# Optimization experiments

Measured on AMD Instinct MI355X. Metric: run time of the kernel, lower is better.

Reference implementation:

```python
import jax, jax.numpy as jnp
import numpy as np

N_EMBD = 1024
N_HEAD = 16
HEAD_DIM = N_EMBD // N_HEAD


def setup_inputs() -> dict:
    key = jax.random.key(0)
    kx, kq, kk, kv, kp = jax.random.split(key, 5)
    B, S = 4, 2048
    x = jax.random.normal(kx, (B, S, N_EMBD), dtype=jnp.float32)
    # nn.Linear(n, n, bias=False): weight [out, in], y = x @ W.T
    s = 1.0 / np.sqrt(N_EMBD)
    Wq = jax.random.uniform(kq, (N_EMBD, N_EMBD), jnp.float32, -s, s)
    Wk = jax.random.uniform(kk, (N_EMBD, N_EMBD), jnp.float32, -s, s)
    Wv = jax.random.uniform(kv, (N_EMBD, N_EMBD), jnp.float32, -s, s)
    Wo = jax.random.uniform(kp, (N_EMBD, N_EMBD), jnp.float32, -s, s)
    return {"x": x, "Wq": Wq, "Wk": Wk, "Wv": Wv, "Wo": Wo}


def _split_heads(t):
    B, S, _ = t.shape
    return t.reshape(B, S, N_HEAD, HEAD_DIM).transpose(0, 2, 1, 3)  # [B,H,S,D]


def reference(x, Wq, Wk, Wv, Wo):
    q = _split_heads(x @ Wq.T)
    k = _split_heads(x @ Wk.T)
    v = _split_heads(x @ Wv.T)
    scale = 1.0 / np.sqrt(HEAD_DIM)
    scores = jnp.einsum('bhqd,bhkd->bhqk', q, k) * scale  # [B,H,S,S]
    S = x.shape[1]
    mask = jnp.tril(jnp.ones((S, S), dtype=bool))
    masked = jnp.where(mask[None, None], scores, -jnp.inf)
    attn = jax.nn.softmax(masked, axis=-1)
    heads = jnp.einsum('bhqk,bhkd->bhqd', attn, v)
    merged = heads.transpose(0, 2, 1, 3).reshape(x.shape[0], S, N_EMBD)
    return merged @ Wo.T
```

## Files before the change

kernel.cpp:

```cpp
#include <hip/hip_runtime.h>
#include <hip/hip_bf16.h>

typedef __hip_bfloat16 bf16;
typedef __attribute__((ext_vector_type(8))) short short8;
typedef __attribute__((ext_vector_type(4))) float f32x4;
typedef unsigned int uint32;

#define MFMA16(a, b, c) __builtin_amdgcn_mfma_f32_16x16x32_bf16(a, b, c, 0, 0, 0)

constexpr int EMB   = 1024;
constexpr int SEQ   = 2048;
constexpr int BATCH = 4;
constexpr int NH    = 16;
constexpr int HD    = 64;
constexpr int QKVW  = 3 * EMB;
constexpr float QSCALE = 0.125f * 1.44269504f;

__device__ __forceinline__ void gl_lds16(const bf16* g, bf16* l) {
    __builtin_amdgcn_global_load_lds(
        (const __attribute__((address_space(1))) void*)g,
        (__attribute__((address_space(3))) void*)l,
        16, 0, 0);
}

__device__ __forceinline__ float fexp2(float x) {
#if __has_builtin(__builtin_amdgcn_exp2f)
    return __builtin_amdgcn_exp2f(x);
#else
    return exp2f(x);
#endif
}

__device__ __forceinline__ uint32 pack2(float a, float b) {
    uint32 ua = __builtin_bit_cast(uint32, a) + 0x8000u;
    uint32 ub = __builtin_bit_cast(uint32, b) + 0x8000u;
    return __builtin_amdgcn_perm(ub, ua, 0x07060302u);
}

__device__ __forceinline__ bf16 fbf16(float f) {
    unsigned short u =
        (unsigned short)((__builtin_bit_cast(uint32, f) + 0x8000u) >> 16);
    return __builtin_bit_cast(bf16, u);
}

__device__ __forceinline__ int ps_dw(int row, int cd) {
    return row * 64 + ((((cd >> 2) ^ (row & 7)) << 3) + ((cd & 3) << 1));
}

__global__ void convert_all(const float* __restrict__ x,
                            const float* __restrict__ wq,
                            const float* __restrict__ wk,
                            const float* __restrict__ wv,
                            const float* __restrict__ wo,
                            bf16* __restrict__ xc,
                            bf16* __restrict__ wqkv,
                            bf16* __restrict__ woc) {
    const int NX = BATCH * SEQ * EMB;
    const int NW = EMB * EMB;
    const float* src; bf16* dst; int n4, b0, nb;
    const int blk = blockIdx.x;
    if (blk < 2048)      { src = x;  dst = xc;          n4 = NX / 4; b0 = 0;    nb = 2048; }
    else if (blk < 2304) { src = wq; dst = wqkv;        n4 = NW / 4; b0 = 2048; nb = 256; }
    else if (blk < 2560) { src = wk; dst = wqkv + NW;   n4 = NW / 4; b0 = 2304; nb = 256; }
    else if (blk < 2816) { src = wv; dst = wqkv + 2*NW; n4 = NW / 4; b0 = 2560; nb = 256; }
    else                 { src = wo; dst = woc;         n4 = NW / 4; b0 = 2816; nb = 256; }
    for (int i = (blk - b0) * 256 + threadIdx.x; i < n4; i += nb * 256) {
        float4 v = ((const float4*)src)[i];
        uint2 o;
        o.x = pack2(v.x, v.y);
        o.y = pack2(v.z, v.w);
        ((uint2*)dst)[i] = o;
    }
}

template <typename OutT>
__global__ __launch_bounds__(256) void gemm_bt(const bf16* __restrict__ A,
                                               const bf16* __restrict__ B,
                                               OutT* __restrict__ C,
                                               int M, int N, int K,
                                               float oscale, int qlim) {
    __shared__ __align__(16) bf16 As[2][128 * 64];
    __shared__ __align__(16) bf16 Bs[2][128 * 64];

    const int t    = threadIdx.x;
    const int lane = t & 63;
    const int wid  = t >> 6;
    const int l16  = lane & 15;
    const int quad = lane >> 4;
    const int e    = l16 & 7;
    const int wm   = (wid >> 1) * 64;
    const int wn   = (wid & 1) * 64;

    const int nwg   = (int)gridDim.x;
    const int cpx   = nwg >> 3;
    const int gx    = N >> 7;
    const int mrows = cpx / gx;
    const int xcd   = (int)blockIdx.x & 7;
    const int local = (int)blockIdx.x >> 3;
    const int m0    = (xcd * mrows + (local % mrows)) * 128;
    const int n0    = (local / mrows) * 128;
    const float sc  = (n0 < qlim) ? oscale : 1.0f;

    f32x4 acc[4][4] = {};
    const int srow = lane >> 3;
    const int scol = ((lane & 7) ^ srow) * 8;

    auto stage = [&](int kt, int buf) {
        const int k0 = kt * 64;
        #pragma unroll
        for (int it = 0; it < 4; ++it) {
            int rb = it * 32 + wid * 8;
            gl_lds16(&A[(size_t)(m0 + rb + srow) * K + k0 + scol], &As[buf][rb * 64]);
            gl_lds16(&B[(size_t)(n0 + rb + srow) * K + k0 + scol], &Bs[buf][rb * 64]);
        }
    };

    const int nk = K >> 6;
    stage(0, 0);
    stage(1, 1);

    for (int kt = 0; kt < nk; ++kt) {
        const int cur = kt & 1;
        if (kt < nk - 1) __builtin_amdgcn_s_waitcnt(0x0F78);
        else             __builtin_amdgcn_s_waitcnt(0x0F70);
        __builtin_amdgcn_s_barrier();

        #pragma unroll
        for (int ks = 0; ks < 64; ks += 32) {
            const int cb = (ks >> 3) + quad;
            short8 af[4], bfr[4];
            #pragma unroll
            for (int i = 0; i < 4; ++i)
                af[i] = *(const short8*)&As[cur][(wm + i * 16 + l16) * 64 + ((cb ^ e) * 8)];
            #pragma unroll
            for (int j = 0; j < 4; ++j)
                bfr[j] = *(const short8*)&Bs[cur][(wn + j * 16 + l16) * 64 + ((cb ^ e) * 8)];
            #pragma unroll
            for (int i = 0; i < 4; ++i)
                #pragma unroll
                for (int j = 0; j < 4; ++j)
                    acc[i][j] = MFMA16(af[i], bfr[j], acc[i][j]);
        }

        __builtin_amdgcn_s_barrier();
        if (kt + 2 < nk) stage(kt + 2, cur);
    }

    #pragma unroll
    for (int i = 0; i < 4; ++i)
        #pragma unroll
        for (int j = 0; j < 4; ++j)
            #pragma unroll
            for (int r = 0; r < 4; ++r) {
                int row = m0 + wm + i * 16 + quad * 4 + r;
                int col = n0 + wn + j * 16 + l16;
                float v = acc[i][j][r] * sc;
                if constexpr (sizeof(OutT) == 2)
                    C[(size_t)row * N + col] = fbf16(v);
                else
                    C[(size_t)row * N + col] = (OutT)v;
            }
}

__global__ __launch_bounds__(256) void transpose_v(const bf16* __restrict__ QKV,
                                                   bf16* __restrict__ Vt) {
    __shared__ __align__(16) bf16 Ts[4096];
    const int t  = threadIdx.x;
    const int st = blockIdx.x;
    const int bh = blockIdx.y;
    const int b  = bh >> 4, h = bh & 15;
    const int s0 = st * 64;

    const bf16* src = QKV + ((size_t)(b * SEQ + s0)) * QKVW + 2 * EMB + h * HD;
    {
        int r = t >> 3, cq = t & 7;
        #pragma unroll
        for (int it = 0; it < 2; ++it, r += 32) {
            uint4 v = *(const uint4*)&src[(size_t)r * QKVW + cq * 8];
            int blk = cq ^ (r >> 3);
            *(uint4*)&Ts[r * 64 + blk * 8] = v;
        }
    }
    __syncthreads();
    bf16* dst = Vt + (size_t)bh * HD * SEQ + s0;
    {
        int d = t >> 3;
        const int sq = t & 7;
        #pragma unroll
        for (int it = 0; it < 2; ++it, d += 32) {
            short8 ov;
            #pragma unroll
            for (int i = 0; i < 8; ++i) {
                int s = sq * 8 + i;
                ov[i] = (short)__bfloat16_as_ushort(
                    Ts[s * 64 + (((d >> 3) ^ sq) << 3) + (d & 7)]);
            }
            *(short8*)&dst[(size_t)d * SEQ + sq * 8] = ov;
        }
    }
}

__global__ __launch_bounds__(256) void flash_attn(const bf16* __restrict__ QKV,
                                                  const bf16* __restrict__ Vt,
                                                  bf16* __restrict__ O) {
    __shared__ __align__(16) bf16 Ks[2][64 * 64];
    __shared__ __align__(16) bf16 VTs[2][64 * 64];
    __shared__ __align__(16) bf16 Ps[4][16 * 64];

    const int t    = threadIdx.x;
    const int lane = t & 63;
    const int w    = t >> 6;
    const int l16  = lane & 15;
    const int quad = lane >> 4;
    const int e    = l16 & 7;

    const int lin = (int)blockIdx.x;
    const int wg  = ((lin & 7) << 7) + (lin >> 3);
    const int bh  = wg >> 4;
    const int pr  = wg & 15;
    const int b   = bh >> 4, h = bh & 15;

    const bf16* Qp = QKV + (size_t)b * SEQ * QKVW + h * HD;
    const bf16* Kp = QKV + (size_t)b * SEQ * QKVW + EMB + h * HD;
    const bf16* Vp = Vt + (size_t)bh * HD * SEQ;
    bf16* Op = O + (size_t)b * SEQ * EMB + h * HD;

    const int srow = lane >> 3;
    const int scol = ((lane & 7) ^ srow) * 8;

    auto stage = [&](int kt, int buf) {
        const int kbase = kt * 64;
        #pragma unroll
        for (int it = 0; it < 2; ++it) {
            int rb = it * 32 + w * 8;
            gl_lds16(&Kp[(size_t)(kbase + rb + srow) * QKVW + scol], &Ks[buf][rb * 64]);
            gl_lds16(&Vp[(size_t)(rb + srow) * SEQ + kbase + scol], &VTs[buf][rb * 64]);
        }
    };

    for (int pass = 0; pass < 2; ++pass) {
        const int qt = pass ? pr : 31 - pr;
        const int q0 = qt * 64;
        const int wq0 = q0 + w * 16;

        short8 bQ[2];
        {
            const size_t qr = (size_t)(wq0 + l16) * QKVW;
            bQ[0] = *(const short8*)&Qp[qr + quad * 8];
            bQ[1] = *(const short8*)&Qp[qr + 32 + quad * 8];
        }

        f32x4 o[4] = {};
        float lrow = 0.f;

        const int ntiles = qt + 1;

        stage(0, 0);
        if (ntiles > 1) stage(1, 1);

        for (int kt = 0; kt < ntiles; ++kt) {
            const int cur = kt & 1;
            const int kbase = kt * 64;
            if (kt < ntiles - 1) __builtin_amdgcn_s_waitcnt(0x0F74);
            else                 __builtin_amdgcn_s_waitcnt(0x0F70);
            __builtin_amdgcn_s_barrier();

            f32x4 sa[4];
            #pragma unroll
            for (int j = 0; j < 4; ++j) {
                f32x4 acc = {};
                acc = MFMA16(*(const short8*)&Ks[cur][(j * 16 + l16) * 64 + ((quad ^ e) * 8)],
                             bQ[0], acc);
                acc = MFMA16(*(const short8*)&Ks[cur][(j * 16 + l16) * 64 + (((4 + quad) ^ e) * 8)],
                             bQ[1], acc);
                sa[j] = acc;
            }

            float lsum = 0.f;
            if (kbase + 63 > wq0) {
                #pragma unroll
                for (int j = 0; j < 4; ++j)
                    #pragma unroll
                    for (int pp = 0; pp < 2; ++pp) {
                        int kg = kbase + j * 16 + quad * 4 + 2 * pp;
                        float e0 = fexp2(sa[j][2 * pp]);
                        float e1 = fexp2(sa[j][2 * pp + 1]);
                        float p0 = (kg     <= wq0 + l16) ? e0 : 0.f;
                        float p1 = (kg + 1 <= wq0 + l16) ? e1 : 0.f;
                        lsum += p0 + p1;
                        *(uint32*)&Ps[w][ps_dw(l16, j * 8 + quad * 2 + pp)] = pack2(p0, p1);
                    }
            } else {
                #pragma unroll
                for (int j = 0; j < 4; ++j)
                    #pragma unroll
                    for (int pp = 0; pp < 2; ++pp) {
                        float p0 = fexp2(sa[j][2 * pp]);
                        float p1 = fexp2(sa[j][2 * pp + 1]);
                        lsum += p0 + p1;
                        *(uint32*)&Ps[w][ps_dw(l16, j * 8 + quad * 2 + pp)] = pack2(p0, p1);
                    }
            }
            lrow += lsum;

            #pragma unroll
            for (int ks = 0; ks < 2; ++ks) {
                short8 bP = *(const short8*)&Ps[w][l16 * 64 + (((ks * 4 + quad) ^ e) << 3)];
                #pragma unroll
                for (int dg = 0; dg < 4; ++dg)
                    o[dg] = MFMA16(
                        *(const short8*)&VTs[cur][(dg * 16 + l16) * 64 + (((ks * 4 + quad) ^ e) * 8)],
                        bP, o[dg]);
            }

            __builtin_amdgcn_s_barrier();
            if (kt + 2 < ntiles) stage(kt + 2, cur);
        }

        {
            float l = lrow;
            l += __shfl_xor(l, 16);
            l += __shfl_xor(l, 32);
            float rl = 1.0f / l;
            #pragma unroll
            for (int dg = 0; dg < 4; ++dg)
                #pragma unroll
                for (int pp = 0; pp < 2; ++pp) {
                    float v0 = o[dg][2 * pp] * rl;
                    float v1 = o[dg][2 * pp + 1] * rl;
                    *(uint32*)&Ps[w][ps_dw(l16, dg * 8 + quad * 2 + pp)] = pack2(v0, v1);
                }
            #pragma unroll
            for (int it = 0; it < 2; ++it) {
                int qr = lane >> 2;
                int ch = (lane & 3) + 4 * it;
                short8 vv = *(const short8*)&Ps[w][qr * 64 + ((ch ^ (qr & 7)) << 3)];
                *(short8*)&Op[(size_t)(wq0 + qr) * EMB + ch * 8] = vv;
            }
        }
    }
}

extern "C" void kernel_launch(void* const* d_in, const int* in_sizes, int n_in,
                              void* d_out, int out_size, void* d_ws, size_t ws_size,
                              hipStream_t stream) {
    const float* x  = (const float*)d_in[0];
    const float* Wq = (const float*)d_in[1];
    const float* Wk = (const float*)d_in[2];
    const float* Wv = (const float*)d_in[3];
    const float* Wo = (const float*)d_in[4];
    float* out = (float*)d_out;
    bf16*  ws  = (bf16*)d_ws;

    const int M  = BATCH * SEQ;
    const int NX = M * EMB;
    const int NW = EMB * EMB;

    bf16* xc   = ws;
    bf16* Ab   = xc;
    bf16* Wqkv = ws + (size_t)NX;
    bf16* Woc  = Wqkv + 3 * (size_t)NW;
    bf16* QKV  = Woc + NW;
    bf16* Vt   = QKV + (size_t)M * QKVW;

    convert_all<<<3072, 256, 0, stream>>>(x, Wq, Wk, Wv, Wo, xc, Wqkv, Woc);

    gemm_bt<bf16><<<dim3((QKVW / 128) * (M / 128)), 256, 0, stream>>>(
        xc, Wqkv, QKV, M, QKVW, EMB, QSCALE, EMB);

    transpose_v<<<dim3(SEQ / 64, BATCH * NH), 256, 0, stream>>>(QKV, Vt);

    flash_attn<<<dim3((SEQ / 64 / 2) * BATCH * NH), 256, 0, stream>>>(QKV, Vt, Ab);

    gemm_bt<float><<<dim3((EMB / 128) * (M / 128)), 256, 0, stream>>>(
        Ab, Woc, out, M, EMB, EMB, 1.0f, 0);
}
```

Before: 237.9 us.

## Split flash attention work across waves by key slice with cross-wave reduction

Result: slower. 245.9 us (+3.4%).

```diff
diff --git a/kernel.cpp b/kernel.cpp
--- a/kernel.cpp
+++ b/kernel.cpp
@@ -3,10 +3,20 @@
 
 typedef __hip_bfloat16 bf16;
 typedef __attribute__((ext_vector_type(8))) short short8;
+typedef __attribute__((ext_vector_type(4))) short short4v;
 typedef __attribute__((ext_vector_type(4))) float f32x4;
 typedef unsigned int uint32;
 
 #define MFMA16(a, b, c) __builtin_amdgcn_mfma_f32_16x16x32_bf16(a, b, c, 0, 0, 0)
+
+__device__ __forceinline__ f32x4 MFMA16K16(short4v a, short4v b, f32x4 c) {
+#if __has_builtin(__builtin_amdgcn_mfma_f32_16x16x16bf16_1k)
+    return __builtin_amdgcn_mfma_f32_16x16x16bf16_1k(a, b, c, 0, 0, 0);
+#else
+    asm("v_mfma_f32_16x16x16_bf16 %0, %1, %2, %0" : "+v"(c) : "v"(a), "v"(b));
+    return c;
+#endif
+}
 
 constexpr int EMB   = 1024;
 constexpr int SEQ   = 2048;
@@ -41,10 +51,6 @@
     unsigned short u =
         (unsigned short)((__builtin_bit_cast(uint32, f) + 0x8000u) >> 16);
     return __builtin_bit_cast(bf16, u);
-}
-
-__device__ __forceinline__ int ps_dw(int row, int cd) {
-    return row * 64 + ((((cd >> 2) ^ (row & 7)) << 3) + ((cd & 3) << 1));
 }
 
 __global__ void convert_all(const float* __restrict__ x,
@@ -200,12 +206,14 @@
     }
 }
 
-__global__ __launch_bounds__(256) void flash_attn(const bf16* __restrict__ QKV,
-                                                  const bf16* __restrict__ Vt,
-                                                  bf16* __restrict__ O) {
-    __shared__ __align__(16) bf16 Ks[2][64 * 64];
-    __shared__ __align__(16) bf16 VTs[2][64 * 64];
-    __shared__ __align__(16) bf16 Ps[4][16 * 64];
+__global__ __launch_bounds__(256, 2) void flash_attn(const bf16* __restrict__ QKV,
+                                                     const bf16* __restrict__ Vt,
+                                                     bf16* __restrict__ O) {
+    __shared__ __align__(16) float smemF[16896];
+    bf16* Ks  = (bf16*)smemF;
+    bf16* VTs = (bf16*)smemF + 8192;
+    constexpr int OF0  = 12480;
+    constexpr int LRED = 16640;
 
     const int t    = threadIdx.x;
     const int lane = t & 63;
@@ -213,11 +221,12 @@
     const int l16  = lane & 15;
     const int quad = lane >> 4;
     const int e    = l16 & 7;
+    const int w16k = w * 16;
 
     const int lin = (int)blockIdx.x;
-    const int wg  = ((lin & 7) << 7) + (lin >> 3);
-    const int bh  = wg >> 4;
-    const int pr  = wg & 15;
+    const int wg  = ((lin & 7) << 6) + (lin >> 3);
+    const int bh  = wg >> 3;
+    const int g   = wg & 7;
     const int b   = bh >> 4, h = bh & 15;
 
     const bf16* Qp = QKV + (size_t)b * SEQ * QKVW + h * HD;
@@ -233,25 +242,29 @@
         #pragma unroll
         for (int it = 0; it < 2; ++it) {
             int rb = it * 32 + w * 8;
-            gl_lds16(&Kp[(size_t)(kbase + rb + srow) * QKVW + scol], &Ks[buf][rb * 64]);
-            gl_lds16(&Vp[(size_t)(rb + srow) * SEQ + kbase + scol], &VTs[buf][rb * 64]);
+            gl_lds16(&Kp[(size_t)(kbase + rb + srow) * QKVW + scol], &Ks[buf * 4096 + rb * 64]);
+            gl_lds16(&Vp[(size_t)(rb + srow) * SEQ + kbase + scol], &VTs[buf * 4096 + rb * 64]);
         }
     };
 
-    for (int pass = 0; pass < 2; ++pass) {
-        const int qt = pass ? pr : 31 - pr;
+    for (int pass = 0; pass < 4; ++pass) {
+        int qt;
+        if      (pass == 0) qt = 31 - g;
+        else if (pass == 1) qt = 16 + g;
+        else if (pass == 2) qt = 15 - g;
+        else                qt = g;
         const int q0 = qt * 64;
-        const int wq0 = q0 + w * 16;
-
-        short8 bQ[2];
-        {
-            const size_t qr = (size_t)(wq0 + l16) * QKVW;
-            bQ[0] = *(const short8*)&Qp[qr + quad * 8];
-            bQ[1] = *(const short8*)&Qp[qr + 32 + quad * 8];
-        }
-
-        f32x4 o[4] = {};
-        float lrow = 0.f;
+
+        short8 bQ[4][2];
+        #pragma unroll
+        for (int qg = 0; qg < 4; ++qg) {
+            const size_t qr = (size_t)(q0 + qg * 16 + l16) * QKVW;
+            bQ[qg][0] = *(const short8*)&Qp[qr + quad * 8];
+            bQ[qg][1] = *(const short8*)&Qp[qr + 32 + quad * 8];
+        }
+
+        f32x4 o[4][4] = {};
+        float lrow[4] = {0.f, 0.f, 0.f, 0.f};
 
         const int ntiles = qt + 1;
 
@@ -265,79 +278,113 @@
             else                 __builtin_amdgcn_s_waitcnt(0x0F70);
             __builtin_amdgcn_s_barrier();
 
-            f32x4 sa[4];
-            #pragma unroll
-            for (int j = 0; j < 4; ++j) {
+            const bf16* Kb = &Ks[cur * 4096];
+            const short8 kf0 = *(const short8*)&Kb[(w16k + l16) * 64 + ((quad ^ e) * 8)];
+            const short8 kf1 = *(const short8*)&Kb[(w16k + l16) * 64 + (((4 + quad) ^ e) * 8)];
+
+            short4v pb[4];
+            const bool diag = (kt == ntiles - 1);
+            const int kgb = kbase + w16k + quad * 4;
+            #pragma unroll
+            for (int qg = 0; qg < 4; ++qg) {
                 f32x4 acc = {};
-                acc = MFMA16(*(const short8*)&Ks[cur][(j * 16 + l16) * 64 + ((quad ^ e) * 8)],
-                             bQ[0], acc);
-                acc = MFMA16(*(const short8*)&Ks[cur][(j * 16 + l16) * 64 + (((4 + quad) ^ e) * 8)],
-                             bQ[1], acc);
-                sa[j] = acc;
-            }
-
-            float lsum = 0.f;
-            if (kbase + 63 > wq0) {
+                acc = MFMA16(kf0, bQ[qg][0], acc);
+                acc = MFMA16(kf1, bQ[qg][1], acc);
+                float p0 = fexp2(acc[0]);
+                float p1 = fexp2(acc[1]);
+                float p2 = fexp2(acc[2]);
+                float p3 = fexp2(acc[3]);
+                if (diag) {
+                    const int qglob = q0 + qg * 16 + l16;
+                    if (kgb     > qglob) p0 = 0.f;
+                    if (kgb + 1 > qglob) p1 = 0.f;
+                    if (kgb + 2 > qglob) p2 = 0.f;
+                    if (kgb + 3 > qglob) p3 = 0.f;
+                }
+                lrow[qg] += (p0 + p1) + (p2 + p3);
+                uint2 u;
+                u.x = pack2(p0, p1);
+                u.y = pack2(p2, p3);
+                pb[qg] = __builtin_bit_cast(short4v, u);
+            }
+
+            const bf16* Vb = &VTs[cur * 4096];
+            #pragma unroll
+            for (int dg = 0; dg < 4; ++dg) {
+                const short4v vf = *(const short4v*)&Vb[(dg * 16 + l16) * 64 +
+                    (((2 * w + (quad >> 1)) ^ e) * 8) + (quad & 1) * 4];
                 #pragma unroll
-                for (int j = 0; j < 4; ++j)
-                    #pragma unroll
-                    for (int pp = 0; pp < 2; ++pp) {
-                        int kg = kbase + j * 16 + quad * 4 + 2 * pp;
-                        float e0 = fexp2(sa[j][2 * pp]);
-                        float e1 = fexp2(sa[j][2 * pp + 1]);
-                        float p0 = (kg     <= wq0 + l16) ? e0 : 0.f;
-                        float p1 = (kg + 1 <= wq0 + l16) ? e1 : 0.f;
-                        lsum += p0 + p1;
-                        *(uint32*)&Ps[w][ps_dw(l16, j * 8 + quad * 2 + pp)] = pack2(p0, p1);
-                    }
-            } else {
-                #pragma unroll
-                for (int j = 0; j < 4; ++j)
-                    #pragma unroll
-                    for (int pp = 0; pp < 2; ++pp) {
-                        float p0 = fexp2(sa[j][2 * pp]);
-                        float p1 = fexp2(sa[j][2 * pp + 1]);
-                        lsum += p0 + p1;
-                        *(uint32*)&Ps[w][ps_dw(l16, j * 8 + quad * 2 + pp)] = pack2(p0, p1);
-                    }
-            }
-            lrow += lsum;
-
-            #pragma unroll
-            for (int ks = 0; ks < 2; ++ks) {
-                short8 bP = *(const short8*)&Ps[w][l16 * 64 + (((ks * 4 + quad) ^ e) << 3)];
-                #pragma unroll
-                for (int dg = 0; dg < 4; ++dg)
-                    o[dg] = MFMA16(
-                        *(const short8*)&VTs[cur][(dg * 16 + l16) * 64 + (((ks * 4 + quad) ^ e) * 8)],
-                        bP, o[dg]);
+                for (int qg = 0; qg < 4; ++qg)
+                    o[dg][qg] = MFMA16K16(vf, pb[qg], o[dg][qg]);
             }
 
             __builtin_amdgcn_s_barrier();
             if (kt + 2 < ntiles) stage(kt + 2, cur);
         }
 
-        {
-            float l = lrow;
+        #pragma unroll
+        for (int qg = 0; qg < 4; ++qg) {
+            float l = lrow[qg];
             l += __shfl_xor(l, 16);
             l += __shfl_xor(l, 32);
-            float rl = 1.0f / l;
-            #pragma unroll
-            for (int dg = 0; dg < 4; ++dg)
+            lrow[qg] = l;
+        }
+        if (quad == 0) {
+            #pragma unroll
+            for (int qg = 0; qg < 4; ++qg)
+                smemF[LRED + w * 64 + qg * 16 + l16] = lrow[qg];
+        }
+        #pragma unroll
+        for (int dg = 0; dg < 4; ++dg) {
+            if (dg == w) continue;
+            const int slot = dg * 3 + (w < dg ? w : w - 1);
+            float* pf = smemF + slot * 1040 + quad * 4 * 65 + l16;
+            #pragma unroll
+            for (int r = 0; r < 4; ++r)
                 #pragma unroll
-                for (int pp = 0; pp < 2; ++pp) {
-                    float v0 = o[dg][2 * pp] * rl;
-                    float v1 = o[dg][2 * pp + 1] * rl;
-                    *(uint32*)&Ps[w][ps_dw(l16, dg * 8 + quad * 2 + pp)] = pack2(v0, v1);
-                }
-            #pragma unroll
-            for (int it = 0; it < 2; ++it) {
-                int qr = lane >> 2;
-                int ch = (lane & 3) + 4 * it;
-                short8 vv = *(const short8*)&Ps[w][qr * 64 + ((ch ^ (qr & 7)) << 3)];
-                *(short8*)&Op[(size_t)(wq0 + qr) * EMB + ch * 8] = vv;
-            }
-        }
+                for (int qg = 0; qg < 4; ++qg)
+                    pf[r * 65 + qg * 16] = o[dg][qg][r];
+        }
+        __syncthreads();
+        #pragma unroll
+        for (int dg = 0; dg < 4; ++dg) {
+            if (dg != w) continue;
+            #pragma unroll
+            for (int s = 0; s < 3; ++s) {
+                const float* pf = smemF + (dg * 3 + s) * 1040 + quad * 4 * 65 + l16;
+                #pragma unroll
+                for (int r = 0; r < 4; ++r)
+                    #pragma unroll
+                    for (int qg = 0; qg < 4; ++qg)
+                        o[dg][qg][r] += pf[r * 65 + qg * 16];
+            }
+            float rlq[4];
+            #pragma unroll
+            for (int qg = 0; qg < 4; ++qg) {
+                float s0 = smemF[LRED +       qg * 16 + l16]
+                         + smemF[LRED +  64 + qg * 16 + l16]
+                         + smemF[LRED + 128 + qg * 16 + l16]
+                         + smemF[LRED + 192 + qg * 16 + l16];
+                rlq[qg] = 1.0f / s0;
+            }
+            float* Of = smemF + OF0 + w * 1040;
+            #pragma unroll
+            for (int r = 0; r < 4; ++r)
+                #pragma unroll
+                for (int qg = 0; qg < 4; ++qg)
+                    Of[(quad * 4 + r) * 65 + qg * 16 + l16] = o[dg][qg][r] * rlq[qg];
+            float f[16];
+            #pragma unroll
+            for (int d = 0; d < 16; ++d) f[d] = Of[d * 65 + lane];
+            uint4 ua, ub;
+            ua.x = pack2(f[0],  f[1]);  ua.y = pack2(f[2],  f[3]);
+            ua.z = pack2(f[4],  f[5]);  ua.w = pack2(f[6],  f[7]);
+            ub.x = pack2(f[8],  f[9]);  ub.y = pack2(f[10], f[11]);
+            ub.z = pack2(f[12], f[13]); ub.w = pack2(f[14], f[15]);
+            *(uint4*)&Op[(size_t)(q0 + lane) * EMB + w16k]     = ua;
+            *(uint4*)&Op[(size_t)(q0 + lane) * EMB + w16k + 8] = ub;
+        }
+        __syncthreads();
     }
 }
 
@@ -370,7 +417,7 @@
 
     transpose_v<<<dim3(SEQ / 64, BATCH * NH), 256, 0, stream>>>(QKV, Vt);
 
-    flash_attn<<<dim3((SEQ / 64 / 2) * BATCH * NH), 256, 0, stream>>>(QKV, Vt, Ab);
+    flash_attn<<<dim3(512), 256, 0, stream>>>(QKV, Vt, Ab);
 
     gemm_bt<float><<<dim3((EMB / 128) * (M / 128)), 256, 0, stream>>>(
         Ab, Woc, out, M, EMB, EMB, 1.0f, 0);
```
